# Kernel tuning notes

Measured on AMD Instinct MI355X. Metric: run time of the kernel, lower is better.

## Reference

```python
import jax, jax.numpy as jnp
import numpy as np

K_NN = 5
COS_EPS = 1e-8  # torch cosine_similarity eps


def setup_inputs() -> dict:
    key = jax.random.key(0)
    ks = jax.random.split(key, 10)
    N1, N2, D, E, H = 2000, 2000, 63, 64, 8
    return {
        "lm_X": jax.random.normal(ks[0], (N1, D), jnp.float32),
        "lm_Y": jax.random.normal(ks[1], (N1, 2), jnp.float32),
        "tg_X": jax.random.normal(ks[2], (N2, D), jnp.float32),
        "tg_Y": jax.random.normal(ks[3], (N2, 2), jnp.float32),
        "lm_delay": jax.random.uniform(ks[4], (N1,), jnp.float32),
        "tg_delay": jax.random.uniform(ks[5], (N2,), jnp.float32),
        # learned params: embedding Linear(input_dim=D+1 -> E) and per-head score weights
        "W_emb": jax.random.normal(ks[6], (E, D + 1), jnp.float32) / np.sqrt(D + 1),
        "b_emb": jnp.zeros((E,), jnp.float32),
        "w1": jax.random.normal(ks[7], (E, H), jnp.float32),
        "w2": jax.random.normal(ks[8], (E, H), jnp.float32),
    }


def _knn_adj(X, k):
    # binary row-wise k-nearest-neighbour adjacency, self excluded
    n = X.shape[0]
    sq = jnp.sum(X * X, axis=1)
    d2 = sq[:, None] + sq[None, :] - 2.0 * (X @ X.T)  # [n, n] squared distances
    d2 = jnp.where(jnp.eye(n, dtype=bool), jnp.inf, d2)  # exclude self
    _, idx = jax.lax.top_k(-d2, k)  # k smallest distances -> [n, k]
    rows = jnp.arange(n)[:, None]
    return jnp.zeros((n, n), X.dtype).at[rows, idx].set(1.0)


def reference(lm_X, lm_Y, tg_X, tg_Y, lm_delay, tg_delay, W_emb, b_emb, w1, w2):
    N1 = lm_X.shape[0]
    N2 = tg_X.shape[0]
    N = N1 + N2
    k = K_NN

    # ---- community-KNN adjacency over landmarks, label aggregation ----
    adj_lm = _knn_adj(lm_X, k)                      # [N1, N1] binary, k ones per row
    y_pred = (adj_lm @ lm_Y) * (1.0 / k)            # [N1, 2]

    # ---- teacher adjacency: (1 - I) with lm block = adj_lm, tg block = 0 ----
    adj_teacher = 1.0 - jnp.eye(N, dtype=lm_X.dtype)
    adj_teacher = adj_teacher.at[:N1, :N1].set(adj_lm)
    adj_teacher = adj_teacher.at[N1:, N1:].set(0.0)

    # ---- node features + embedding ----
    lm_feat = jnp.concatenate([lm_X, lm_delay[:, None]], axis=1)  # [N1, D+1]
    tg_feat = jnp.concatenate([tg_X, tg_delay[:, None]], axis=1)  # [N2, D+1]
    feats = jnp.concatenate([lm_feat, tg_feat], axis=0)           # [N, D+1]
    e = feats @ W_emb.T + b_emb                                    # [N, E]

    # ---- multi-head cosine-similarity edge probabilities (all heads at once) ----
    a = e[:, None, :] * w1.T[None, :, :]            # [N, H, E] : e * w1[:, h]
    b = e[:, None, :] * w2.T[None, :, :]            # [N, H, E] : e * w2[:, h]
    na = jnp.linalg.norm(a, axis=-1)                # [N, H]
    nb = jnp.linalg.norm(b, axis=-1)                # [N, H]
    dot = jnp.einsum("nhe,mhe->nmh", a, b)          # [N, N, H]
    sim = dot / jnp.maximum(na[:, None, :] * nb[None, :, :], COS_EPS)
    alpha = jax.nn.sigmoid(sim)                      # [N, N, H]
    adj = jnp.mean(alpha, axis=-1)                   # [N, N]

    return (y_pred, adj, adj_teacher)
```

## Files before the change

kernel.cpp:

```cpp
#include <hip/hip_runtime.h>
#include <math.h>

#define N1 2000
#define N2 2000
#define NT 4000
#define D  63
#define E  64
#define H  8
#define KNN 5
#define NPAD 4032
#define MPAD 4096

typedef short bf16x8 __attribute__((ext_vector_type(8)));
typedef float f32x4  __attribute__((ext_vector_type(4)));

__device__ __forceinline__ unsigned short f2bf(float x) {
    unsigned u = __float_as_uint(x);
    u = (u + 0x7fffu + ((u >> 16) & 1u)) >> 16;
    return (unsigned short)u;
}

__global__ void k_sq(const float* __restrict__ X, float* __restrict__ sq) {
    int i = blockIdx.x * blockDim.x + threadIdx.x;
    if (i < N1) {
        float s = 0.f;
        for (int d = 0; d < D; ++d) { float v = X[i * D + d]; s += v * v; }
        sq[i] = s;
    }
}

__global__ __launch_bounds__(256) void k_d2(const float* __restrict__ X,
                                            const float* __restrict__ sq,
                                            float* __restrict__ d2) {
    __shared__ float Xi[64][68];
    __shared__ float Xj[64][68];
    int i0 = blockIdx.y * 64, j0 = blockIdx.x * 64;
    int tid = threadIdx.x;
    for (int t = tid; t < 64 * 64; t += 256) {
        int r = t >> 6, c = t & 63;
        int gi = min(i0 + r, N1 - 1);
        int gj = min(j0 + r, N1 - 1);
        Xi[r][c] = (c < D) ? X[gi * D + c] : 0.f;
        Xj[r][c] = (c < D) ? X[gj * D + c] : 0.f;
    }
    __syncthreads();
    int tx = tid & 15, ty = tid >> 4;
    float acc[4][4];
    #pragma unroll
    for (int a = 0; a < 4; ++a)
        #pragma unroll
        for (int b = 0; b < 4; ++b) acc[a][b] = 0.f;

    #pragma unroll 4
    for (int kk = 0; kk < 16; ++kk) {
        float4 av[4], bv[4];
        #pragma unroll
        for (int ii = 0; ii < 4; ++ii) av[ii] = *(const float4*)&Xi[ty + 16 * ii][4 * kk];
        #pragma unroll
        for (int jj = 0; jj < 4; ++jj) bv[jj] = *(const float4*)&Xj[tx + 16 * jj][4 * kk];
        #pragma unroll
        for (int ii = 0; ii < 4; ++ii)
            #pragma unroll
            for (int jj = 0; jj < 4; ++jj)
                acc[ii][jj] += av[ii].x * bv[jj].x + av[ii].y * bv[jj].y +
                               av[ii].z * bv[jj].z + av[ii].w * bv[jj].w;
    }

    #pragma unroll
    for (int ii = 0; ii < 4; ++ii) {
        int i = i0 + ty + 16 * ii;
        #pragma unroll
        for (int jj = 0; jj < 4; ++jj) {
            int j = j0 + tx + 16 * jj;
            if (i < N1 && j < N1) {
                float v = sq[i] + sq[j] - 2.f * acc[ii][jj];
                if (i == j) v = __builtin_inff();
                d2[i * N1 + j] = v;
            }
        }
    }
}

__device__ __forceinline__ bool dless(float d1, int i1, float d2v, int i2) {
    return d1 < d2v || (d1 == d2v && i1 < i2);
}

__device__ __forceinline__ void ins5(float bd[KNN], int bi[KNN], float d, int j) {
    if (dless(d, j, bd[KNN - 1], bi[KNN - 1])) {
        bd[KNN - 1] = d; bi[KNN - 1] = j;
        #pragma unroll
        for (int s = KNN - 1; s > 0; --s) {
            if (dless(bd[s], bi[s], bd[s - 1], bi[s - 1])) {
                float td = bd[s]; bd[s] = bd[s - 1]; bd[s - 1] = td;
                int ti = bi[s]; bi[s] = bi[s - 1]; bi[s - 1] = ti;
            }
        }
    }
}

__global__ __launch_bounds__(256) void k_top5(const float* __restrict__ d2,
                                              const float* __restrict__ lmY,
                                              float* __restrict__ ypred,
                                              int* __restrict__ idx) {
    __shared__ float sd[4 * KNN];
    __shared__ int   si[4 * KNN];
    int i = blockIdx.x;
    int tid = threadIdx.x;
    const float* row = d2 + i * N1;

    float bd[KNN]; int bi[KNN];
    #pragma unroll
    for (int s = 0; s < KNN; ++s) { bd[s] = __builtin_inff(); bi[s] = 0x7fffffff; }
    #pragma unroll
    for (int k = 0; k < 8; ++k) {
        int j = tid + k * 256;
        if (j < N1) ins5(bd, bi, row[j], j);
    }

    int lane = tid & 63, wave = tid >> 6;
    float wd[KNN]; int wi[KNN];
    #pragma unroll
    for (int s = 0; s < KNN; ++s) {
        float d = bd[0]; int ix = bi[0];
        #pragma unroll
        for (int m = 1; m < 64; m <<= 1) {
            float od = __shfl_xor(d, m, 64);
            int   oi = __shfl_xor(ix, m, 64);
            if (dless(od, oi, d, ix)) { d = od; ix = oi; }
        }
        wd[s] = d; wi[s] = ix;
        if (d == bd[0] && ix == bi[0]) {
            #pragma unroll
            for (int q = 0; q < KNN - 1; ++q) { bd[q] = bd[q + 1]; bi[q] = bi[q + 1]; }
            bd[KNN - 1] = __builtin_inff(); bi[KNN - 1] = 0x7fffffff;
        }
    }
    if (lane == 0) {
        #pragma unroll
        for (int s = 0; s < KNN; ++s) { sd[wave * KNN + s] = wd[s]; si[wave * KNN + s] = wi[s]; }
    }
    __syncthreads();
    if (wave == 0) {
        float d = (lane < 4 * KNN) ? sd[lane] : __builtin_inff();
        int  ix = (lane < 4 * KNN) ? si[lane] : 0x7fffffff;
        float rd[KNN]; int ri[KNN];
        #pragma unroll
        for (int s = 0; s < KNN; ++s) {
            float md = d; int mi = ix;
            #pragma unroll
            for (int m = 1; m < 64; m <<= 1) {
                float od = __shfl_xor(md, m, 64);
                int   oi = __shfl_xor(mi, m, 64);
                if (dless(od, oi, md, mi)) { md = od; mi = oi; }
            }
            rd[s] = md; ri[s] = mi;
            if (md == d && mi == ix) { d = __builtin_inff(); ix = 0x7fffffff; }
        }
        if (lane == 0) {
            float y0 = 0.f, y1 = 0.f;
            #pragma unroll
            for (int s = 0; s < KNN; ++s) {
                int j = ri[s];
                y0 += lmY[j * 2];
                y1 += lmY[j * 2 + 1];
                idx[i * KNN + s] = j;
            }
            ypred[i * 2]     = y0 * 0.2f;
            ypred[i * 2 + 1] = y1 * 0.2f;
        }
    }
}

__global__ __launch_bounds__(256) void k_prep(const float* __restrict__ lmX,
                                              const float* __restrict__ tgX,
                                              const float* __restrict__ lmD,
                                              const float* __restrict__ tgD,
                                              const float* __restrict__ W,
                                              const float* __restrict__ bias,
                                              const float* __restrict__ w1,
                                              const float* __restrict__ w2,
                                              unsigned short* __restrict__ AL,
                                              unsigned short* __restrict__ Bbuf,
                                              float* __restrict__ sB) {
    __shared__ float f[4][E];
    __shared__ float Wl[E][68];
    int tid = threadIdx.x, lane = tid & 63, wave = tid >> 6;
    int n = blockIdx.x * 4 + wave;
    #pragma unroll
    for (int k = 0; k < 4; ++k) {
        int g = k * 256 + tid;
        float4 v = ((const float4*)W)[g];
        int r = g >> 4, c = (g & 15) * 4;
        *(float4*)&Wl[r][c] = v;
    }
    int t = lane;
    if (t < D)  f[wave][t] = (n < N1) ? lmX[n * D + t] : tgX[(n - N1) * D + t];
    if (t == D) f[wave][t] = (n < N1) ? lmD[n] : tgD[n - N1];
    __syncthreads();
    float s0 = 0.f, s1 = 0.f, s2 = 0.f, s3 = 0.f;
    #pragma unroll
    for (int k = 0; k < 16; ++k) {
        float4 wv = *(const float4*)&Wl[t][4 * k];
        float4 fv = *(const float4*)&f[wave][4 * k];
        s0 += fv.x * wv.x; s1 += fv.y * wv.y; s2 += fv.z * wv.z; s3 += fv.w * wv.w;
    }
    const float en = bias[t] + (s0 + s1) + (s2 + s3);
    Bbuf[n * E + t] = f2bf(en);

    int kc = t >> 5, kq = (t >> 3) & 3, j = t & 7;
    int alane = kq * 16 + (n & 15);
    int nb = n >> 4;
    #pragma unroll
    for (int h = 0; h < H; ++h) {
        float a = en * w1[t * H + h];
        float b = en * w2[t * H + h];
        float na2 = a * a, nb2 = b * b;
        #pragma unroll
        for (int m = 32; m >= 1; m >>= 1) {
            na2 += __shfl_xor(na2, m, 64);
            nb2 += __shfl_xor(nb2, m, 64);
        }
        float val = a * w2[t * H + h] * rsqrtf(na2);
        AL[(((nb * 8 + h) << 1) + kc) * 512 + alane * 8 + j] = f2bf(val);
        if (t == h) sB[n * H + h] = rsqrtf(nb2);
    }
}

__global__ __launch_bounds__(256) void k_adjm(const unsigned short* __restrict__ AL,
                                              const unsigned short* __restrict__ Bbuf,
                                              const float* __restrict__ sB,
                                              const int* __restrict__ idx,
                                              float* __restrict__ adj,
                                              float* __restrict__ adjT) {
    __shared__ unsigned short Bt[256][68];
    int tid = threadIdx.x;
    int m0 = blockIdx.x * 256, n0 = blockIdx.y * 64;

    #pragma unroll
    for (int it = 0; it < 8; ++it) {
        int g = it * 256 + tid;
        int row = g >> 3, c = g & 7;
        *(bf16x8*)&Bt[row][c * 8] = *(const bf16x8*)&Bbuf[(m0 + row) * E + c * 8];
    }

    int wave = tid >> 6, lane = tid & 63;
    int l15 = lane & 15, kq = lane >> 4;
    int nb = blockIdx.y * 4 + wave;

    bf16x8 afr[H][2];
    #pragma unroll
    for (int h = 0; h < H; ++h)
        #pragma unroll
        for (int kc = 0; kc < 2; ++kc)
            afr[h][kc] = *(const bf16x8*)&AL[(((nb * 8 + h) << 1) + kc) * 512 + lane * 8];

    __syncthreads();

    int nebase = n0 + wave * 16 + kq * 4;

    #pragma unroll 2
    for (int mt = 0; mt < 16; ++mt) {
        int mrow = mt * 16 + l15;
        int mcol = m0 + mrow;
        bf16x8 b0 = *(const bf16x8*)&Bt[mrow][kq * 8];
        bf16x8 b1 = *(const bf16x8*)&Bt[mrow][32 + kq * 8];

        float sbv[H];
        *(f32x4*)&sbv[0] = *(const f32x4*)&sB[mcol * H + 0];
        *(f32x4*)&sbv[4] = *(const f32x4*)&sB[mcol * H + 4];

        f32x4 acc[H];
        #pragma unroll
        for (int h = 0; h < H; ++h) {
            acc[h] = (f32x4){0.f, 0.f, 0.f, 0.f};
            acc[h] = __builtin_amdgcn_mfma_f32_16x16x32_bf16(afr[h][0], b0, acc[h], 0, 0, 0);
            acc[h] = __builtin_amdgcn_mfma_f32_16x16x32_bf16(afr[h][1], b1, acc[h], 0, 0, 0);
        }

        bool mok = (mcol < NT);
        #pragma unroll
        for (int reg = 0; reg < 4; ++reg) {
            int ne = nebase + reg;
            float sum = 0.f;
            #pragma unroll
            for (int h = 0; h < H; ++h) {
                float x = acc[h][reg] * sbv[h];
                float u = x * x;
                float p = fmaf(u, 1.8919e-3f, -2.0833333e-2f);
                p = fmaf(u, p, 0.25f);
                sum = fmaf(x, p, sum);
            }
            if (mok && ne < NT) adj[ne * NT + mcol] = fmaf(sum, 0.125f, 0.5f);
        }
    }

    #pragma unroll
    for (int it = 0; it < 16; ++it) {
        int g = it * 256 + tid;
        int r = g >> 6;
        int col = m0 + (g & 63) * 4;
        int row = n0 + r;
        if (row < NT && col < NT) {
            float v = ((row < N1) != (col < N1)) ? 1.f : 0.f;
            float4 o = {v, v, v, v};
            *(float4*)&adjT[row * NT + col] = o;
        }
    }
    __syncthreads();
    for (int p = tid; p < 64 * KNN; p += 256) {
        int r = p / KNN, s = p - r * KNN;
        int row = n0 + r;
        if (row < N1) {
            int jx = idx[row * KNN + s];
            if (jx >= m0 && jx < m0 + 256) adjT[row * NT + jx] = 1.f;
        }
    }
}

extern "C" void kernel_launch(void* const* d_in, const int* in_sizes, int n_in,
                              void* d_out, int out_size, void* d_ws, size_t ws_size,
                              hipStream_t stream) {
    const float* lmX  = (const float*)d_in[0];
    const float* lmY  = (const float*)d_in[1];
    const float* tgX  = (const float*)d_in[2];
    const float* lmD  = (const float*)d_in[4];
    const float* tgD  = (const float*)d_in[5];
    const float* Wemb = (const float*)d_in[6];
    const float* bemb = (const float*)d_in[7];
    const float* w1   = (const float*)d_in[8];
    const float* w2   = (const float*)d_in[9];

    float* out   = (float*)d_out;
    float* ypred = out;
    float* adj   = out + 4000;
    float* adjT  = out + 4000 + 16000000;

    char* ws = (char*)d_ws;
    unsigned short* AL   = (unsigned short*)ws;
    unsigned short* Bbuf = (unsigned short*)(ws + 4128768);
    float*          sB   = (float*)(ws + 4128768 + 524288);
    float*          sq   = (float*)(ws + 4784128);
    int*            idx  = (int*)  (ws + 4792128);

    float* d2 = adj;

    k_sq<<<(N1 + 255) / 256, 256, 0, stream>>>(lmX, sq);
    dim3 g2((N1 + 63) / 64, (N1 + 63) / 64);
    k_d2<<<g2, 256, 0, stream>>>(lmX, sq, d2);
    k_top5<<<N1, 256, 0, stream>>>(d2, lmY, ypred, idx);
    k_prep<<<NT / 4, 256, 0, stream>>>(lmX, tgX, lmD, tgD, Wemb, bemb, w1, w2,
                                       AL, Bbuf, sB);
    dim3 ga(MPAD / 256, NPAD / 64);
    k_adjm<<<ga, 256, 0, stream>>>(AL, Bbuf, sB, idx, adj, adjT);
}
```

Baseline: 226.0 us.

## Fuse squared-norm into distance kernel and interleave teacher stores with MFMA loop

Removes the separate k_sq launch by computing row squared norms from the shared-memory tiles inside k_d2. In k_adjm, the B-fragment LDS reads are double-buffered across m-tiles, the teacher-adjacency stores are moved into the main MFMA loop so they overlap compute, the LDS row pitch is changed, and an occupancy hint is added to launch bounds. These changes aim to cut launch overhead and hide store latency, at the cost of higher register pressure and possible LDS bank conflicts with the new padding.

```diff
diff --git a/kernel.cpp b/kernel.cpp
--- a/kernel.cpp
+++ b/kernel.cpp
@@ -20,20 +20,11 @@
     return (unsigned short)u;
 }
 
-__global__ void k_sq(const float* __restrict__ X, float* __restrict__ sq) {
-    int i = blockIdx.x * blockDim.x + threadIdx.x;
-    if (i < N1) {
-        float s = 0.f;
-        for (int d = 0; d < D; ++d) { float v = X[i * D + d]; s += v * v; }
-        sq[i] = s;
-    }
-}
-
 __global__ __launch_bounds__(256) void k_d2(const float* __restrict__ X,
-                                            const float* __restrict__ sq,
                                             float* __restrict__ d2) {
     __shared__ float Xi[64][68];
     __shared__ float Xj[64][68];
+    __shared__ float sqi[64], sqj[64];
     int i0 = blockIdx.y * 64, j0 = blockIdx.x * 64;
     int tid = threadIdx.x;
     for (int t = tid; t < 64 * 64; t += 256) {
@@ -44,6 +35,20 @@
         Xj[r][c] = (c < D) ? X[gj * D + c] : 0.f;
     }
     __syncthreads();
+    {
+        int lane = tid & 63, wave = tid >> 6;
+        if (wave < 2) {
+            const float(*Xr)[68] = (wave == 0) ? Xi : Xj;
+            float s = 0.f;
+            #pragma unroll
+            for (int k = 0; k < 16; ++k) {
+                float4 v = *(const float4*)&Xr[lane][4 * k];
+                s += v.x * v.x + v.y * v.y + v.z * v.z + v.w * v.w;
+            }
+            if (wave == 0) sqi[lane] = s; else sqj[lane] = s;
+        }
+    }
+    __syncthreads();
     int tx = tid & 15, ty = tid >> 4;
     float acc[4][4];
     #pragma unroll
@@ -73,7 +78,7 @@
         for (int jj = 0; jj < 4; ++jj) {
             int j = j0 + tx + 16 * jj;
             if (i < N1 && j < N1) {
-                float v = sq[i] + sq[j] - 2.f * acc[ii][jj];
+                float v = sqi[ty + 16 * ii] + sqj[tx + 16 * jj] - 2.f * acc[ii][jj];
                 if (i == j) v = __builtin_inff();
                 d2[i * N1 + j] = v;
             }
@@ -226,13 +231,13 @@
     }
 }
 
-__global__ __launch_bounds__(256) void k_adjm(const unsigned short* __restrict__ AL,
-                                              const unsigned short* __restrict__ Bbuf,
-                                              const float* __restrict__ sB,
-                                              const int* __restrict__ idx,
-                                              float* __restrict__ adj,
-                                              float* __restrict__ adjT) {
-    __shared__ unsigned short Bt[256][68];
+__global__ __launch_bounds__(256, 4) void k_adjm(const unsigned short* __restrict__ AL,
+                                                 const unsigned short* __restrict__ Bbuf,
+                                                 const float* __restrict__ sB,
+                                                 const int* __restrict__ idx,
+                                                 float* __restrict__ adj,
+                                                 float* __restrict__ adjT) {
+    __shared__ unsigned short Bt[256][66];
     int tid = threadIdx.x;
     int m0 = blockIdx.x * 256, n0 = blockIdx.y * 64;
 
@@ -257,17 +262,27 @@
     __syncthreads();
 
     int nebase = n0 + wave * 16 + kq * 4;
-
-    #pragma unroll 2
+    int trow = n0 + wave * 16 + l15;
+    int tcol0 = m0 + (lane >> 4) * 4;
+    bool trowlm = trow < N1;
+    bool trowok = trow < NT;
+
+    bf16x8 b0 = *(const bf16x8*)&Bt[l15][kq * 8];
+    bf16x8 b1 = *(const bf16x8*)&Bt[l15][32 + kq * 8];
+
     for (int mt = 0; mt < 16; ++mt) {
         int mrow = mt * 16 + l15;
         int mcol = m0 + mrow;
-        bf16x8 b0 = *(const bf16x8*)&Bt[mrow][kq * 8];
-        bf16x8 b1 = *(const bf16x8*)&Bt[mrow][32 + kq * 8];
 
         float sbv[H];
         *(f32x4*)&sbv[0] = *(const f32x4*)&sB[mcol * H + 0];
         *(f32x4*)&sbv[4] = *(const f32x4*)&sB[mcol * H + 4];
+
+        bf16x8 nb0, nb1;
+        if (mt < 15) {
+            nb0 = *(const bf16x8*)&Bt[mrow + 16][kq * 8];
+            nb1 = *(const bf16x8*)&Bt[mrow + 16][32 + kq * 8];
+        }
 
         f32x4 acc[H];
         #pragma unroll
@@ -275,6 +290,15 @@
             acc[h] = (f32x4){0.f, 0.f, 0.f, 0.f};
             acc[h] = __builtin_amdgcn_mfma_f32_16x16x32_bf16(afr[h][0], b0, acc[h], 0, 0, 0);
             acc[h] = __builtin_amdgcn_mfma_f32_16x16x32_bf16(afr[h][1], b1, acc[h], 0, 0, 0);
+        }
+
+        {
+            int col = tcol0 + mt * 16;
+            if (trowok && col < NT) {
+                float v = (trowlm != (col < N1)) ? 1.f : 0.f;
+                float4 o = {v, v, v, v};
+                *(float4*)&adjT[trow * NT + col] = o;
+            }
         }
 
         bool mok = (mcol < NT);
@@ -292,20 +316,10 @@
             }
             if (mok && ne < NT) adj[ne * NT + mcol] = fmaf(sum, 0.125f, 0.5f);
         }
-    }
-
-    #pragma unroll
-    for (int it = 0; it < 16; ++it) {
-        int g = it * 256 + tid;
-        int r = g >> 6;
-        int col = m0 + (g & 63) * 4;
-        int row = n0 + r;
-        if (row < NT && col < NT) {
-            float v = ((row < N1) != (col < N1)) ? 1.f : 0.f;
-            float4 o = {v, v, v, v};
-            *(float4*)&adjT[row * NT + col] = o;
-        }
-    }
+
+        b0 = nb0; b1 = nb1;
+    }
+
     __syncthreads();
     for (int p = tid; p < 64 * KNN; p += 256) {
         int r = p / KNN, s = p - r * KNN;
@@ -339,14 +353,12 @@
     unsigned short* AL   = (unsigned short*)ws;
     unsigned short* Bbuf = (unsigned short*)(ws + 4128768);
     float*          sB   = (float*)(ws + 4128768 + 524288);
-    float*          sq   = (float*)(ws + 4784128);
-    int*            idx  = (int*)  (ws + 4792128);
+    int*            idx  = (int*)  (ws + 4784128);
 
     float* d2 = adj;
 
-    k_sq<<<(N1 + 255) / 256, 256, 0, stream>>>(lmX, sq);
     dim3 g2((N1 + 63) / 64, (N1 + 63) / 64);
-    k_d2<<<g2, 256, 0, stream>>>(lmX, sq, d2);
+    k_d2<<<g2, 256, 0, stream>>>(lmX, d2);
     k_top5<<<N1, 256, 0, stream>>>(d2, lmY, ypred, idx);
     k_prep<<<NT / 4, 256, 0, stream>>>(lmX, tgX, lmD, tgD, Wemb, bemb, w1, w2,
                                        AL, Bbuf, sB);
```

New measurement: 227.6 us. No clear change (+0.7%).
